# Kernel optimization log

Hardware: AMD Instinct MI355X
Metric: run time of the kernel (lower is better)

## Reference

```python
import jax, jax.numpy as jnp
import numpy as np

D_MODEL = 1024
N_HEADS = 16
HEAD_DIM = D_MODEL // N_HEADS


def setup_inputs() -> dict:
    key = jax.random.key(0)
    ks = jax.random.split(key, 5)
    s = 1.0 / np.sqrt(D_MODEL)
    return {
        "x": jax.random.normal(ks[0], (2, 2048, D_MODEL), dtype=jnp.float32),
        "w_qkv": jax.random.uniform(ks[1], (3 * D_MODEL, D_MODEL), jnp.float32, -s, s),
        "b_qkv": jax.random.uniform(ks[2], (3 * D_MODEL,), jnp.float32, -s, s),
        "w_out": jax.random.uniform(ks[3], (D_MODEL, D_MODEL), jnp.float32, -s, s),
        "b_out": jax.random.uniform(ks[4], (D_MODEL,), jnp.float32, -s, s),
    }


def _attn(x, w_qkv, b_qkv, w_out, b_out):
    bsz, seq_len, _ = x.shape
    qkv = jnp.einsum('bsd,ed->bse', x, w_qkv) + b_qkv  # [B,S,3D]
    q, k, v = jnp.split(qkv, 3, axis=-1)
    def heads(t):  # [B,S,D] -> [B,H,S,Dh]
        return t.reshape(bsz, seq_len, N_HEADS, HEAD_DIM).transpose(0, 2, 1, 3)
    q, k, v = heads(q), heads(k), heads(v)
    scores = jnp.einsum('bhqd,bhkd->bhqk', q, k) / np.sqrt(HEAD_DIM)
    mask = jnp.tril(jnp.ones((seq_len, seq_len), dtype=bool))
    scores = jnp.where(mask, scores, -jnp.inf)
    probs = jax.nn.softmax(scores, axis=-1)
    attn = jnp.einsum('bhqk,bhkd->bhqd', probs, v)
    attn = attn.transpose(0, 2, 1, 3).reshape(bsz, seq_len, D_MODEL)
    return jnp.einsum('bsd,ed->bse', attn, w_out) + b_out


def reference(x, w_qkv, b_qkv, w_out, b_out):
    return _attn(x, w_qkv, b_qkv, w_out, b_out)
```

## Files before the change

### kernel.cpp

```cpp
#include <hip/hip_runtime.h>
#include <hip/hip_bf16.h>
#include <stdint.h>

#define SEQ     2048
#define BATCH   2
#define NHEADS  16
#define HDIM    64
#define DMODEL  1024
#define N3      3072
#define D2      2048
#define MTOT    (BATCH*SEQ)

typedef __attribute__((ext_vector_type(4))) float f32x4;
typedef __attribute__((ext_vector_type(8))) short bf16x8;

static __device__ inline unsigned short f2bf(float f) {
    union { float f; unsigned u; } v; v.f = f;
    unsigned r = (v.u + 0x7fffu + ((v.u >> 16) & 1u)) >> 16;
    return (unsigned short)r;
}
static __device__ inline unsigned pk2bf(float a, float b) {
    union { __hip_bfloat162 h; unsigned u; } c;
    c.h = __float22bfloat162_rn(make_float2(a, b));
    return c.u;
}

#define GLDS(gp, lp) __builtin_amdgcn_global_load_lds( \
    (const __attribute__((address_space(1))) void*)(gp), \
    (__attribute__((address_space(3))) void*)(lp), 16, 0, 0)

__global__ void cast_all(const float* __restrict__ x,
                         const float* __restrict__ wqkv,
                         const float* __restrict__ wout,
                         unsigned short* __restrict__ xb,
                         unsigned short* __restrict__ wqkvb,
                         unsigned short* __restrict__ woutb) {
    long i4 = (long)(blockIdx.x * blockDim.x + threadIdx.x) * 4;
    const float* src; unsigned short* dst; long off;
    if (i4 < 4194304L)      { src = x;    dst = xb;    off = i4; }
    else if (i4 < 7340032L) { src = wqkv; dst = wqkvb; off = i4 - 4194304L; }
    else                    { src = wout; dst = woutb; off = i4 - 7340032L; }
    float4 v = *(const float4*)(src + off);
    union { uint2 u; ushort4 s; } pk;
    pk.u.x = pk2bf(v.x, v.y); pk.u.y = pk2bf(v.z, v.w);
    *(ushort4*)(dst + off) = pk.s;
}

__global__ __launch_bounds__(512, 1) void gemm_qkv(
    const unsigned short* __restrict__ A,
    const unsigned short* __restrict__ B,
    const float* __restrict__ bias,
    unsigned short* __restrict__ qk,
    unsigned short* __restrict__ vT)
{
    __shared__ __align__(16) unsigned short sA[2][256][64];
    __shared__ __align__(16) unsigned short sB[2][256][64];
    const int tid  = threadIdx.x;
    const int w    = tid >> 6, lane = tid & 63;
    const int quad = lane >> 4, l16 = lane & 15, l7 = l16 & 7;
    const int wm = w >> 2, wn = w & 3;
    const int bid = blockIdx.x;
    const int m0 = (bid & 15) << 8;
    const int n0 = (bid >> 4) << 8;

    f32x4 acc[8][4];
    const f32x4 zero = {0.f, 0.f, 0.f, 0.f};
    #pragma unroll
    for (int i = 0; i < 8; i++)
        #pragma unroll
        for (int j = 0; j < 4; j++) acc[i][j] = zero;

    const int rsel = tid >> 3;
    const int sgl  = (tid & 7) ^ (rsel & 7);
    const unsigned short* gA = A + (long)(m0 + rsel) * 1024 + sgl * 8;
    const unsigned short* gB = B + (long)(n0 + rsel) * 1024 + sgl * 8;

    #pragma unroll
    for (int j = 0; j < 4; j++) {
        GLDS(gA + (long)(64 * j) * 1024, &sA[0][64 * j + w * 8][0]);
        GLDS(gB + (long)(64 * j) * 1024, &sB[0][64 * j + w * 8][0]);
    }

    auto compute_tile = [&](const unsigned short (*A_)[64],
                            const unsigned short (*B_)[64]) {
        #pragma unroll
        for (int mh = 0; mh < 2; mh++) {
            bf16x8 af[4][2];
            #pragma unroll
            for (int mt2 = 0; mt2 < 4; mt2++)
                #pragma unroll
                for (int kk = 0; kk < 2; kk++)
                    af[mt2][kk] = *(const bf16x8*)(
                        &A_[wm * 128 + mh * 64 + mt2 * 16 + l16]
                           [(((kk << 2) + quad) ^ l7) * 8]);
            #pragma unroll
            for (int nh = 0; nh < 2; nh++) {
                bf16x8 bfr[2][2];
                #pragma unroll
                for (int nt2 = 0; nt2 < 2; nt2++)
                    #pragma unroll
                    for (int kk = 0; kk < 2; kk++)
                        bfr[nt2][kk] = *(const bf16x8*)(
                            &B_[wn * 64 + nh * 32 + nt2 * 16 + l16]
                               [(((kk << 2) + quad) ^ l7) * 8]);
                #pragma unroll
                for (int mt2 = 0; mt2 < 4; mt2++)
                    #pragma unroll
                    for (int nt2 = 0; nt2 < 2; nt2++)
                        #pragma unroll
                        for (int kk = 0; kk < 2; kk++)
                            acc[mh * 4 + mt2][nh * 2 + nt2] =
                                __builtin_amdgcn_mfma_f32_16x16x32_bf16(
                                    af[mt2][kk], bfr[nt2][kk],
                                    acc[mh * 4 + mt2][nh * 2 + nt2], 0, 0, 0);
            }
        }
    };

    for (int t = 0; t < 15; ++t) {
        const int nb = (t + 1) & 1, cb = t & 1;
        const long ko = (long)(t + 1) * 64;
        #pragma unroll
        for (int j = 0; j < 4; j++) {
            GLDS(gA + (long)(64 * j) * 1024 + ko, &sA[nb][64 * j + w * 8][0]);
            GLDS(gB + (long)(64 * j) * 1024 + ko, &sB[nb][64 * j + w * 8][0]);
        }
        __builtin_amdgcn_sched_barrier(0);
        asm volatile("s_waitcnt vmcnt(8)" ::: "memory");
        __builtin_amdgcn_sched_barrier(0);
        __builtin_amdgcn_s_barrier();
        compute_tile(sA[cb], sB[cb]);
        asm volatile("s_waitcnt lgkmcnt(0)" ::: "memory");
        __builtin_amdgcn_sched_barrier(0);
        __builtin_amdgcn_s_barrier();
    }
    asm volatile("s_waitcnt vmcnt(0)" ::: "memory");
    __builtin_amdgcn_sched_barrier(0);
    __builtin_amdgcn_s_barrier();
    compute_tile(sA[1], sB[1]);

    if (n0 < 2048) {
        #pragma unroll
        for (int nt = 0; nt < 4; nt++) {
            const int n_g = n0 + wn * 64 + nt * 16 + l16;
            const float bv = bias[n_g];
            #pragma unroll
            for (int mt = 0; mt < 8; mt++) {
                #pragma unroll
                for (int r = 0; r < 4; r++) {
                    const int m_g = m0 + wm * 128 + mt * 16 + quad * 4 + r;
                    qk[(long)m_g * D2 + n_g] = f2bf(acc[mt][nt][r] + bv);
                }
            }
        }
    } else {
        const int b = m0 >> 11;
        #pragma unroll
        for (int nt = 0; nt < 4; nt++) {
            const int n_g = n0 + wn * 64 + nt * 16 + l16;
            const int dm = n_g - 2048;
            const long vrow = (long)(((b << 4) + (dm >> 6)) << 6) + (dm & 63);
            const float bv = bias[n_g];
            #pragma unroll
            for (int mt = 0; mt < 8; mt++) {
                const int m_g = m0 + wm * 128 + mt * 16 + quad * 4;
                union { uint2 u; ushort4 s; } pk;
                pk.u.x = pk2bf(acc[mt][nt][0] + bv, acc[mt][nt][1] + bv);
                pk.u.y = pk2bf(acc[mt][nt][2] + bv, acc[mt][nt][3] + bv);
                *(ushort4*)(vT + vrow * D2 + (m_g & 2047)) = pk.s;
            }
        }
    }
}

__global__ __launch_bounds__(256, 2) void gemm_out(
    const unsigned short* __restrict__ A,
    const unsigned short* __restrict__ B,
    const float* __restrict__ bias,
    float* __restrict__ C)
{
    __shared__ __align__(16) unsigned short sA[2][128][64];
    __shared__ __align__(16) unsigned short sB[2][64][64];
    const int tid  = threadIdx.x;
    const int wave = tid >> 6, lane = tid & 63;
    const int quad = lane >> 4, l16 = lane & 15, l7 = l16 & 7;
    const int wm = wave >> 1, wn = wave & 1;
    const int m0 = blockIdx.x * 128, n0 = blockIdx.y * 64;

    f32x4 acc[4][2];
    const f32x4 zero = {0.f, 0.f, 0.f, 0.f};
    #pragma unroll
    for (int i = 0; i < 4; i++) { acc[i][0] = zero; acc[i][1] = zero; }

    const int rsel = tid >> 3;
    const int sgl  = (tid & 7) ^ (rsel & 7);
    const unsigned short* gA0 = A + (long)(m0 + rsel) * 1024 + sgl * 8;
    const unsigned short* gB0 = B + (long)(n0 + rsel) * 1024 + sgl * 8;

    #pragma unroll
    for (int i = 0; i < 4; i++)
        GLDS(gA0 + (long)(32 * i) * 1024, &sA[0][32 * i + wave * 8][0]);
    #pragma unroll
    for (int i = 0; i < 2; i++)
        GLDS(gB0 + (long)(32 * i) * 1024, &sB[0][32 * i + wave * 8][0]);

    int buf = 0;
    for (int k0 = 0; k0 < 1024; k0 += 64, buf ^= 1) {
        __syncthreads();
        if (k0 + 64 < 1024) {
            #pragma unroll
            for (int i = 0; i < 4; i++)
                GLDS(gA0 + (long)(32 * i) * 1024 + k0 + 64, &sA[buf ^ 1][32 * i + wave * 8][0]);
            #pragma unroll
            for (int i = 0; i < 2; i++)
                GLDS(gB0 + (long)(32 * i) * 1024 + k0 + 64, &sB[buf ^ 1][32 * i + wave * 8][0]);
        }
        #pragma unroll
        for (int ks = 0; ks < 2; ks++) {
            bf16x8 af[4], bfr[2];
            #pragma unroll
            for (int mt = 0; mt < 4; mt++)
                af[mt] = *(const bf16x8*)(&sA[buf][wm * 64 + mt * 16 + l16][((ks * 4 + quad) ^ l7) * 8]);
            #pragma unroll
            for (int nt = 0; nt < 2; nt++)
                bfr[nt] = *(const bf16x8*)(&sB[buf][wn * 32 + nt * 16 + l16][((ks * 4 + quad) ^ l7) * 8]);
            #pragma unroll
            for (int mt = 0; mt < 4; mt++)
                #pragma unroll
                for (int nt = 0; nt < 2; nt++)
                    acc[mt][nt] = __builtin_amdgcn_mfma_f32_16x16x32_bf16(
                        af[mt], bfr[nt], acc[mt][nt], 0, 0, 0);
        }
    }
    #pragma unroll
    for (int nt = 0; nt < 2; nt++) {
        const int n_g = n0 + wn * 32 + nt * 16 + l16;
        const float bv = bias[n_g];
        #pragma unroll
        for (int mt = 0; mt < 4; mt++) {
            #pragma unroll
            for (int r = 0; r < 4; r++) {
                const int m_g = m0 + wm * 64 + mt * 16 + quad * 4 + r;
                C[(long)m_g * DMODEL + n_g] = acc[mt][nt][r] + bv;
            }
        }
    }
}

__global__ __launch_bounds__(256, 2) void attn_kernel(
    const unsigned short* __restrict__ qk,
    const unsigned short* __restrict__ vT,
    unsigned short* __restrict__ attn)
{
    __shared__ __align__(16) unsigned short sK [2][2][64][64];
    __shared__ __align__(16) unsigned short sVt[2][2][64][64];
    __shared__ __align__(16) unsigned short sP [4][16][64];

    const int tid  = threadIdx.x;
    const int w    = tid >> 6, lane = tid & 63;
    const int quad = lane >> 4, l16 = lane & 15, l7 = l16 & 7;

    const int bh = blockIdx.x;
    const int b  = bh >> 4, h = bh & 15;
    const int pair = blockIdx.y;
    const long rowb = (long)b * SEQ;

    const int rl = lane >> 3;
    const int sm = (lane & 7) ^ rl;
    const unsigned short* kg = qk + (rowb + w * 16 + rl) * D2 + 1024 + h * HDIM + sm * 8;
    const unsigned short* vg = vT + (long)(bh * 64 + w * 16 + rl) * D2 + sm * 8;

    const int s0 = quad ^ l7;
    const float C2 = 0.18033688011112042f;
    const f32x4 zero = {0.f, 0.f, 0.f, 0.f};

    #pragma unroll
    for (int ph = 0; ph < 2; ph++) {
        const int qtile  = ph ? (31 - pair) : pair;
        const int qbase  = qtile * 64;
        const int ntiles = qtile + 1;
        const int npairs = (ntiles + 1) >> 1;

        bf16x8 qf0, qf1;
        {
            const unsigned short* qp = qk + (rowb + qbase + w * 16 + l16) * D2 + h * HDIM;
            qf0 = *(const bf16x8*)(qp + quad * 8);
            qf1 = *(const bf16x8*)(qp + 32 + quad * 8);
        }
        f32x4 Oacc[4];
        #pragma unroll
        for (int mf = 0; mf < 4; mf++) Oacc[mf] = zero;
        float l_i = 0.f;

        __syncthreads();
        {
            const long o0 = 0, o1 = (long)(1 <= qtile ? 1 : qtile) * 64;
            GLDS(kg + o0 * D2,           &sK [0][0][w * 16][0]);
            GLDS(kg + o0 * D2 + 8L * D2, &sK [0][0][w * 16 + 8][0]);
            GLDS(vg + o0,                &sVt[0][0][w * 16][0]);
            GLDS(vg + o0 + 8L * D2,      &sVt[0][0][w * 16 + 8][0]);
            GLDS(kg + o1 * D2,           &sK [0][1][w * 16][0]);
            GLDS(kg + o1 * D2 + 8L * D2, &sK [0][1][w * 16 + 8][0]);
            GLDS(vg + o1,                &sVt[0][1][w * 16][0]);
            GLDS(vg + o1 + 8L * D2,      &sVt[0][1][w * 16 + 8][0]);
        }

        int buf = 0;
        for (int p = 0; p < npairs; p++, buf ^= 1) {
            __syncthreads();
            if (p + 1 < npairs) {
                const int t0 = 2 * p + 2, t1 = 2 * p + 3;
                const long o0 = (long)(t0 <= qtile ? t0 : qtile) * 64;
                const long o1 = (long)(t1 <= qtile ? t1 : qtile) * 64;
                GLDS(kg + o0 * D2,           &sK [buf ^ 1][0][w * 16][0]);
                GLDS(kg + o0 * D2 + 8L * D2, &sK [buf ^ 1][0][w * 16 + 8][0]);
                GLDS(vg + o0,                &sVt[buf ^ 1][0][w * 16][0]);
                GLDS(vg + o0 + 8L * D2,      &sVt[buf ^ 1][0][w * 16 + 8][0]);
                GLDS(kg + o1 * D2,           &sK [buf ^ 1][1][w * 16][0]);
                GLDS(kg + o1 * D2 + 8L * D2, &sK [buf ^ 1][1][w * 16 + 8][0]);
                GLDS(vg + o1,                &sVt[buf ^ 1][1][w * 16][0]);
                GLDS(vg + o1 + 8L * D2,      &sVt[buf ^ 1][1][w * 16 + 8][0]);
            }
            #pragma unroll
            for (int s = 0; s < 2; s++) {
                const int t = 2 * p + s;
                if (t >= ntiles) break;

                f32x4 st[4];
                #pragma unroll
                for (int kvf = 0; kvf < 4; kvf++) {
                    bf16x8 kf0 = *(const bf16x8*)(&sK[buf][s][kvf * 16 + l16][s0 * 8]);
                    bf16x8 kf1 = *(const bf16x8*)(&sK[buf][s][kvf * 16 + l16][(s0 ^ 4) * 8]);
                    st[kvf] = __builtin_amdgcn_mfma_f32_16x16x32_bf16(kf0, qf0, zero, 0, 0, 0);
                    st[kvf] = __builtin_amdgcn_mfma_f32_16x16x32_bf16(kf1, qf1, st[kvf], 0, 0, 0);
                }
                if (t == qtile) {
                    const int ql = w * 16 + l16;
                    #pragma unroll
                    for (int kvf = 0; kvf < 4; kvf++) {
                        const int kv = kvf * 16 + quad * 4;
                        #pragma unroll
                        for (int r = 0; r < 4; r++)
                            if (kv + r > ql) st[kvf][r] = -1e30f;
                    }
                }
                #pragma unroll
                for (int kvf = 0; kvf < 4; kvf++) {
                    #pragma unroll
                    for (int r = 0; r < 4; r++)
                        st[kvf][r] = __builtin_amdgcn_exp2f(st[kvf][r] * C2);
                }
                f32x4 ps = (st[0] + st[1]) + (st[2] + st[3]);
                l_i += (ps[0] + ps[1]) + (ps[2] + ps[3]);

                #pragma unroll
                for (int kvf = 0; kvf < 4; kvf++) {
                    union { uint2 u; ushort4 s4; } pk;
                    pk.u.x = pk2bf(st[kvf][0], st[kvf][1]);
                    pk.u.y = pk2bf(st[kvf][2], st[kvf][3]);
                    const int seg = (kvf * 2 + (quad >> 1)) ^ l7;
                    *(ushort4*)(&sP[w][l16][seg * 8 + (quad & 1) * 4]) = pk.s4;
                }
                bf16x8 pf0 = *(const bf16x8*)(&sP[w][l16][(quad ^ l7) * 8]);
                bf16x8 pf1 = *(const bf16x8*)(&sP[w][l16][((4 + quad) ^ l7) * 8]);
                #pragma unroll
                for (int mf = 0; mf < 4; mf++) {
                    bf16x8 vf0 = *(const bf16x8*)(&sVt[buf][s][mf * 16 + l16][s0 * 8]);
                    bf16x8 vf1 = *(const bf16x8*)(&sVt[buf][s][mf * 16 + l16][(s0 ^ 4) * 8]);
                    Oacc[mf] = __builtin_amdgcn_mfma_f32_16x16x32_bf16(vf0, pf0, Oacc[mf], 0, 0, 0);
                    Oacc[mf] = __builtin_amdgcn_mfma_f32_16x16x32_bf16(vf1, pf1, Oacc[mf], 0, 0, 0);
                }
            }
        }
        float L = l_i;
        L += __shfl_xor(L, 16);
        L += __shfl_xor(L, 32);
        const float inv = 1.0f / L;
        const int q = qbase + w * 16 + l16;
        unsigned short* op = attn + (rowb + q) * DMODEL + h * HDIM + quad * 4;
        #pragma unroll
        for (int mf = 0; mf < 4; mf++) {
            union { uint2 u; ushort4 s4; } pk;
            pk.u.x = pk2bf(Oacc[mf][0] * inv, Oacc[mf][1] * inv);
            pk.u.y = pk2bf(Oacc[mf][2] * inv, Oacc[mf][3] * inv);
            *(ushort4*)(op + mf * 16) = pk.s4;
        }
    }
}

extern "C" void kernel_launch(void* const* d_in, const int* in_sizes, int n_in,
                              void* d_out, int out_size, void* d_ws, size_t ws_size,
                              hipStream_t stream) {
    const float* x    = (const float*)d_in[0];
    const float* wqkv = (const float*)d_in[1];
    const float* bqkv = (const float*)d_in[2];
    const float* wout = (const float*)d_in[3];
    const float* bout = (const float*)d_in[4];

    char* ws = (char*)d_ws;
    unsigned short* xb    = (unsigned short*)(ws);
    unsigned short* wqkvb = (unsigned short*)(ws + (8L << 20));
    unsigned short* woutb = (unsigned short*)(ws + (14L << 20));
    unsigned short* qkb   = (unsigned short*)(ws + (16L << 20));
    unsigned short* vTb   = (unsigned short*)(ws + (32L << 20));
    unsigned short* attnb = (unsigned short*)(ws + (40L << 20));

    cast_all<<<8192, 256, 0, stream>>>(x, wqkv, wout, xb, wqkvb, woutb);

    gemm_qkv<<<192, 512, 0, stream>>>(xb, wqkvb, bqkv, qkb, vTb);

    dim3 g2(32, 16);
    attn_kernel<<<g2, 256, 0, stream>>>(qkb, vTb, attnb);

    dim3 g3(32, 16);
    gemm_out<<<g3, 256, 0, stream>>>(attnb, woutb, bout, (float*)d_out);
}
```

Baseline: 175.8 us.

## Use 128-row query tiles with 8 waves per block sharing K/V loads

The attention kernel now runs 512 threads (8 waves) per block, each block covering 128 query rows instead of 64, so every K/V tile staged in shared memory serves twice as many queries. The grid shrinks to 32x8 and each wave loads half as many rows per tile. The causal mask now spans the last two KV tiles, and s_setprio is raised around the MFMA sections to favour the matrix work. The costs are lower occupancy (launch bounds 512,1), fewer blocks to hide latency, and some wasted compute on fully masked half tiles.

```diff
diff --git a/kernel.cpp b/kernel.cpp
--- a/kernel.cpp
+++ b/kernel.cpp
@@ -247,14 +247,14 @@
     }
 }
 
-__global__ __launch_bounds__(256, 2) void attn_kernel(
+__global__ __launch_bounds__(512, 1) void attn_kernel(
     const unsigned short* __restrict__ qk,
     const unsigned short* __restrict__ vT,
     unsigned short* __restrict__ attn)
 {
     __shared__ __align__(16) unsigned short sK [2][2][64][64];
     __shared__ __align__(16) unsigned short sVt[2][2][64][64];
-    __shared__ __align__(16) unsigned short sP [4][16][64];
+    __shared__ __align__(16) unsigned short sP [8][16][64];
 
     const int tid  = threadIdx.x;
     const int w    = tid >> 6, lane = tid & 63;
@@ -267,8 +267,8 @@
 
     const int rl = lane >> 3;
     const int sm = (lane & 7) ^ rl;
-    const unsigned short* kg = qk + (rowb + w * 16 + rl) * D2 + 1024 + h * HDIM + sm * 8;
-    const unsigned short* vg = vT + (long)(bh * 64 + w * 16 + rl) * D2 + sm * 8;
+    const unsigned short* kg = qk + (rowb + w * 8 + rl) * D2 + 1024 + h * HDIM + sm * 8;
+    const unsigned short* vg = vT + (long)(bh * 64 + w * 8 + rl) * D2 + sm * 8;
 
     const int s0 = quad ^ l7;
     const float C2 = 0.18033688011112042f;
@@ -276,10 +276,10 @@
 
     #pragma unroll
     for (int ph = 0; ph < 2; ph++) {
-        const int qtile  = ph ? (31 - pair) : pair;
-        const int qbase  = qtile * 64;
-        const int ntiles = qtile + 1;
-        const int npairs = (ntiles + 1) >> 1;
+        const int qtile  = ph ? (15 - pair) : pair;
+        const int qbase  = qtile * 128;
+        const int ntiles = 2 * qtile + 2;
+        const int npairs = ntiles >> 1;
 
         bf16x8 qf0, qf1;
         {
@@ -294,39 +294,29 @@
 
         __syncthreads();
         {
-            const long o0 = 0, o1 = (long)(1 <= qtile ? 1 : qtile) * 64;
-            GLDS(kg + o0 * D2,           &sK [0][0][w * 16][0]);
-            GLDS(kg + o0 * D2 + 8L * D2, &sK [0][0][w * 16 + 8][0]);
-            GLDS(vg + o0,                &sVt[0][0][w * 16][0]);
-            GLDS(vg + o0 + 8L * D2,      &sVt[0][0][w * 16 + 8][0]);
-            GLDS(kg + o1 * D2,           &sK [0][1][w * 16][0]);
-            GLDS(kg + o1 * D2 + 8L * D2, &sK [0][1][w * 16 + 8][0]);
-            GLDS(vg + o1,                &sVt[0][1][w * 16][0]);
-            GLDS(vg + o1 + 8L * D2,      &sVt[0][1][w * 16 + 8][0]);
+            GLDS(kg,            &sK [0][0][w * 8][0]);
+            GLDS(vg,            &sVt[0][0][w * 8][0]);
+            GLDS(kg + 64L * D2, &sK [0][1][w * 8][0]);
+            GLDS(vg + 64,       &sVt[0][1][w * 8][0]);
         }
 
         int buf = 0;
         for (int p = 0; p < npairs; p++, buf ^= 1) {
             __syncthreads();
             if (p + 1 < npairs) {
-                const int t0 = 2 * p + 2, t1 = 2 * p + 3;
-                const long o0 = (long)(t0 <= qtile ? t0 : qtile) * 64;
-                const long o1 = (long)(t1 <= qtile ? t1 : qtile) * 64;
-                GLDS(kg + o0 * D2,           &sK [buf ^ 1][0][w * 16][0]);
-                GLDS(kg + o0 * D2 + 8L * D2, &sK [buf ^ 1][0][w * 16 + 8][0]);
-                GLDS(vg + o0,                &sVt[buf ^ 1][0][w * 16][0]);
-                GLDS(vg + o0 + 8L * D2,      &sVt[buf ^ 1][0][w * 16 + 8][0]);
-                GLDS(kg + o1 * D2,           &sK [buf ^ 1][1][w * 16][0]);
-                GLDS(kg + o1 * D2 + 8L * D2, &sK [buf ^ 1][1][w * 16 + 8][0]);
-                GLDS(vg + o1,                &sVt[buf ^ 1][1][w * 16][0]);
-                GLDS(vg + o1 + 8L * D2,      &sVt[buf ^ 1][1][w * 16 + 8][0]);
+                const long o0 = (long)(2 * p + 2) * 64;
+                const long o1 = (long)(2 * p + 3) * 64;
+                GLDS(kg + o0 * D2, &sK [buf ^ 1][0][w * 8][0]);
+                GLDS(vg + o0,      &sVt[buf ^ 1][0][w * 8][0]);
+                GLDS(kg + o1 * D2, &sK [buf ^ 1][1][w * 8][0]);
+                GLDS(vg + o1,      &sVt[buf ^ 1][1][w * 8][0]);
             }
             #pragma unroll
             for (int s = 0; s < 2; s++) {
                 const int t = 2 * p + s;
-                if (t >= ntiles) break;
 
                 f32x4 st[4];
+                __builtin_amdgcn_s_setprio(1);
                 #pragma unroll
                 for (int kvf = 0; kvf < 4; kvf++) {
                     bf16x8 kf0 = *(const bf16x8*)(&sK[buf][s][kvf * 16 + l16][s0 * 8]);
@@ -334,11 +324,13 @@
                     st[kvf] = __builtin_amdgcn_mfma_f32_16x16x32_bf16(kf0, qf0, zero, 0, 0, 0);
                     st[kvf] = __builtin_amdgcn_mfma_f32_16x16x32_bf16(kf1, qf1, st[kvf], 0, 0, 0);
                 }
-                if (t == qtile) {
+                __builtin_amdgcn_s_setprio(0);
+                if (t >= 2 * qtile) {
                     const int ql = w * 16 + l16;
+                    const int tb = (t - 2 * qtile) * 64;
                     #pragma unroll
                     for (int kvf = 0; kvf < 4; kvf++) {
-                        const int kv = kvf * 16 + quad * 4;
+                        const int kv = tb + kvf * 16 + quad * 4;
                         #pragma unroll
                         for (int r = 0; r < 4; r++)
                             if (kv + r > ql) st[kvf][r] = -1e30f;
@@ -363,6 +355,7 @@
                 }
                 bf16x8 pf0 = *(const bf16x8*)(&sP[w][l16][(quad ^ l7) * 8]);
                 bf16x8 pf1 = *(const bf16x8*)(&sP[w][l16][((4 + quad) ^ l7) * 8]);
+                __builtin_amdgcn_s_setprio(1);
                 #pragma unroll
                 for (int mf = 0; mf < 4; mf++) {
                     bf16x8 vf0 = *(const bf16x8*)(&sVt[buf][s][mf * 16 + l16][s0 * 8]);
@@ -370,6 +363,7 @@
                     Oacc[mf] = __builtin_amdgcn_mfma_f32_16x16x32_bf16(vf0, pf0, Oacc[mf], 0, 0, 0);
                     Oacc[mf] = __builtin_amdgcn_mfma_f32_16x16x32_bf16(vf1, pf1, Oacc[mf], 0, 0, 0);
                 }
+                __builtin_amdgcn_s_setprio(0);
             }
         }
         float L = l_i;
@@ -409,8 +403,8 @@
 
     gemm_qkv<<<192, 512, 0, stream>>>(xb, wqkvb, bqkv, qkb, vTb);
 
-    dim3 g2(32, 16);
-    attn_kernel<<<g2, 256, 0, stream>>>(qkb, vTb, attnb);
+    dim3 g2(32, 8);
+    attn_kernel<<<g2, 512, 0, stream>>>(qkb, vTb, attnb);
 
     dim3 g3(32, 16);
     gemm_out<<<g3, 256, 0, stream>>>(attnb, woutb, bout, (float*)d_out);
```

Result: no change. 174.2 us (-0.9%).
